# Kernel tuning notes

Measured on AMD Instinct MI355X. Metric: run time of the kernel, lower is better.

The kernel has to match this reference:

```python
import jax, jax.numpy as jnp
import numpy as np

B, C, H, W = 8, 512, 64, 64
HID = 4 * C  # MixFFN hidden = in_dim*4
FOCUS = 3.0


def _ln(x, g, b, eps=1e-5):
    m = x.mean(-1, keepdims=True)
    v = ((x - m) ** 2).mean(-1, keepdims=True)
    return (x - m) / jnp.sqrt(v + eps) * g + b


def setup_inputs() -> dict:
    key = jax.random.key(0)
    ks = jax.random.split(key, 12)
    init = lambda k, shape, fan: (jax.random.normal(k, shape, jnp.float32) / np.float32(np.sqrt(fan)))
    d = {}
    d['x'] = jax.random.normal(ks[0], (B, C, H, W), jnp.float32)
    # 1x1 conv weights stored as (Cout, Cin)
    d['Wq'] = init(ks[1], (C, C), C); d['bq'] = jnp.zeros((C,), jnp.float32)
    d['Wk'] = init(ks[2], (C, C), C); d['bk'] = jnp.zeros((C,), jnp.float32)
    d['Wv'] = init(ks[3], (C, C), C); d['bv'] = jnp.zeros((C,), jnp.float32)
    d['scale'] = jnp.zeros((1, 1, C), jnp.float32)  # nn.Parameter(torch.zeros)
    # MixFFN_skip params
    d['fc1_w'] = init(ks[4], (C, HID), C); d['fc1_b'] = jnp.zeros((HID,), jnp.float32)
    d['dw_w'] = init(ks[5], (HID, 1, 3, 3), 9); d['dw_b'] = jnp.zeros((HID,), jnp.float32)
    d['fc2_w'] = init(ks[6], (HID, C), HID); d['fc2_b'] = jnp.zeros((C,), jnp.float32)
    d['ln1_g'] = jnp.ones((HID,), jnp.float32); d['ln1_b'] = jnp.zeros((HID,), jnp.float32)
    d['lnm_g'] = jnp.ones((C,), jnp.float32); d['lnm_b'] = jnp.zeros((C,), jnp.float32)
    return d


def _forward(x, Wq, bq, Wk, bk, Wv, bv, scale, fc1_w, fc1_b, dw_w, dw_b, fc2_w, fc2_b, ln1_g, ln1_b, lnm_g, lnm_b):
    b, c, h, w = x.shape
    n = h * w
    # 1x1 convs (NCHW), then RAW reshape to (B, N, C) as in torch (no permute!)
    conv1 = lambda t, Wm, bm: jnp.einsum('bchw,oc->bohw', t, Wm) + bm[None, :, None, None]
    q = jax.nn.softmax(conv1(x, Wq, bq).reshape(b, n, c), axis=1)
    k = jax.nn.softmax(conv1(x, Wk, bk).reshape(b, n, c), axis=2)
    v = conv1(x, Wv, bv).reshape(b, n, c)
    q = jax.nn.relu(q) + 1e-6
    k = jax.nn.relu(k) + 1e-6
    sc = jax.nn.softplus(scale)
    q = q / sc
    k = k / sc
    q_norm = jnp.linalg.norm(q, axis=-1, keepdims=True)
    k_norm = jnp.linalg.norm(k, axis=-1, keepdims=True)
    q = q ** FOCUS  # focusing_factor <= 6 branch
    k = k ** FOCUS
    q = q / jnp.linalg.norm(q, axis=-1, keepdims=True) * q_norm
    k = k / jnp.linalg.norm(k, axis=-1, keepdims=True) * k_norm
    # num_heads == 1: (b h) n c == b n c
    z = 1.0 / (jnp.einsum('bic,bc->bi', q, k.sum(axis=1)) + 1e-6)
    kv = jnp.einsum('bjc,bjd->bcd', k, v)  # O(N) linear attention summary
    attn = jnp.einsum('bic,bcd,bi->bid', q, kv, z)
    shortcut = jnp.transpose(x, (0, 2, 3, 1)).reshape(b, n, c)  # proper rearrange b c h w -> b (h w) c
    enhanced = shortcut + attn
    # MixFFN_skip(norm_mlp(enhanced), h, w)
    t = _ln(enhanced, lnm_g, lnm_b)
    a = t @ fc1_w + fc1_b  # (B, N, HID)
    ai = jnp.transpose(a, (0, 2, 1)).reshape(b, HID, h, w)
    dw = jax.lax.conv_general_dilated(ai, dw_w, (1, 1), 'SAME',
                                      dimension_numbers=('NCHW', 'OIHW', 'NCHW'),
                                      feature_group_count=HID)
    dw = dw + dw_b[None, :, None, None]
    dw = jnp.transpose(dw.reshape(b, HID, n), (0, 2, 1))
    ax = jax.nn.gelu(_ln(dw + a, ln1_g, ln1_b), approximate=False)
    mlp_out = ax @ fc2_w + fc2_b
    out = enhanced + mlp_out
    return out.reshape(b, h, w, c)


def reference(x, Wq, bq, Wk, bk, Wv, bv, scale, fc1_w, fc1_b, dw_w, dw_b, fc2_w, fc2_b, ln1_g, ln1_b, lnm_g, lnm_b):
    return _forward(x, Wq, bq, Wk, bk, Wv, bv, scale, fc1_w, fc1_b, dw_w, dw_b, fc2_w, fc2_b, ln1_g, ln1_b, lnm_g, lnm_b)
```

## Files before the change

### kernel.cpp

```cpp
#include <hip/hip_runtime.h>
#include <hip/hip_bf16.h>

typedef __hip_bfloat16 bf16;
typedef __attribute__((ext_vector_type(8))) short bh8;
typedef __attribute__((ext_vector_type(4))) short bh4;
typedef __attribute__((ext_vector_type(4))) float f32x4;

#define CDIM 512
#define NDIM 4096
#define HIDD 2048
#define BATCH 8

__device__ __forceinline__ float bf2f(short s) {
    union { unsigned u; float f; } c; c.u = ((unsigned)(unsigned short)s) << 16; return c.f;
}
__device__ __forceinline__ short f2bf(float f) {
    union { __hip_bfloat16 h; short s; } c; c.h = __float2bfloat16(f); return c.s;
}
__device__ __forceinline__ float wsum(float v) {
#pragma unroll
    for (int o = 32; o; o >>= 1) v += __shfl_xor(v, o);
    return v;
}
__device__ __forceinline__ float wmax(float v) {
#pragma unroll
    for (int o = 32; o; o >>= 1) v = fmaxf(v, __shfl_xor(v, o));
    return v;
}

#define GLL(g, l) __builtin_amdgcn_global_load_lds( \
    (const __attribute__((address_space(1))) unsigned int*)(g), \
    (__attribute__((address_space(3))) unsigned int*)(l), 16, 0, 0)

__device__ __forceinline__ void xcd_swz(int& bx, int& by, int& bz) {
    const int gx = gridDim.x, gy = gridDim.y;
    const int nwg = gx * gy * gridDim.z;
    int lid = blockIdx.x + gx * (blockIdx.y + gy * blockIdx.z);
    const int cpx = nwg >> 3;
    int swz = (lid & 7) * cpx + (lid >> 3);
    bx = swz % gx; swz /= gx;
    by = swz % gy;
    bz = swz / gy;
}

enum { EP_QEXP = 0, EP_BF16_BROW = 1, EP_ATTN = 3, EP_BF16_BCOL = 4, EP_OUT = 5 };

template<int MODE, int TM>
__global__ __launch_bounds__(256)
void gemm_bt(const bf16* __restrict__ A, int lda, long sA,
             const bf16* __restrict__ Bt, int ldb, long sB,
             void* __restrict__ Cp, int ldc, long sC, int K,
             const float* __restrict__ bias,
             const float* __restrict__ aux1, long sAux1,
             const float* __restrict__ aux2, long sAux2)
{
    constexpr int MF = TM / 32;
    __shared__ __align__(16) bf16 As[TM * 64];
    __shared__ __align__(16) bf16 Bs[128 * 64];
    int bx, by, bz;
    xcd_swz(bx, by, bz);
    const bf16* Ab = A + (long)bz * sA + (long)by * TM * lda;
    const bf16* Bb = Bt + (long)bz * sB + (long)bx * 128 * ldb;
    const int t = threadIdx.x, lane = t & 63, wid = t >> 6;
    const int wm = wid >> 1, wn = wid & 1, lg = lane >> 4, lr = lane & 15;

    f32x4 acc[MF][4];
#pragma unroll
    for (int m = 0; m < MF; ++m)
#pragma unroll
        for (int n = 0; n < 4; ++n) acc[m][n] = (f32x4){0.f, 0.f, 0.f, 0.f};

    for (int kt = 0; kt < K; kt += 64) {
#pragma unroll
        for (int i = 0; i < MF; ++i) {
            const int ch = i * 256 + t;
            const int row = ch >> 3;
            const int cs = (ch & 7) ^ (row & 7);
            GLL(Ab + (long)row * lda + kt + (cs << 3), (char*)As + i * 4096 + wid * 1024);
        }
#pragma unroll
        for (int i = 0; i < 4; ++i) {
            const int ch = i * 256 + t;
            const int row = ch >> 3;
            const int cs = (ch & 7) ^ (row & 7);
            GLL(Bb + (long)row * ldb + kt + (cs << 3), (char*)Bs + i * 4096 + wid * 1024);
        }
        __syncthreads();
#pragma unroll
        for (int kk = 0; kk < 2; ++kk) {
            bh8 af[MF], bfv[4];
#pragma unroll
            for (int m = 0; m < MF; ++m) {
                const int row = wm * (TM / 2) + m * 16 + lr;
                const int kc = (kk * 4 + lg) ^ (row & 7);
                af[m] = *(const bh8*)(As + row * 64 + kc * 8);
            }
#pragma unroll
            for (int n = 0; n < 4; ++n) {
                const int row = wn * 64 + n * 16 + lr;
                const int kc = (kk * 4 + lg) ^ (row & 7);
                bfv[n] = *(const bh8*)(Bs + row * 64 + kc * 8);
            }
#pragma unroll
            for (int m = 0; m < MF; ++m)
#pragma unroll
                for (int n = 0; n < 4; ++n)
                    acc[m][n] = __builtin_amdgcn_mfma_f32_16x16x32_bf16(af[m], bfv[n], acc[m][n], 0, 0, 0);
        }
        __syncthreads();
    }

    const int gr0 = by * TM + wm * (TM / 2);
    const int gc0 = bx * 128 + wn * 64;
#pragma unroll
    for (int m = 0; m < MF; ++m) {
#pragma unroll
        for (int n = 0; n < 4; ++n) {
            const int gc = gc0 + n * 16 + lr;
#pragma unroll
            for (int r = 0; r < 4; ++r) {
                const int gr = gr0 + m * 16 + lg * 4 + r;
                float v = acc[m][n][r];
                if constexpr (MODE == EP_QEXP) {
                    ((bf16*)Cp + (long)bz * sC)[(long)gr * ldc + gc] = __float2bfloat16(expf(v + bias[gr]));
                } else if constexpr (MODE == EP_BF16_BROW) {
                    ((bf16*)Cp + (long)bz * sC)[(long)gr * ldc + gc] = __float2bfloat16(v + bias[gr]);
                } else if constexpr (MODE == EP_ATTN) {
                    const float* xg = aux1 + (long)bz * sAux1;
                    const float* zg = aux2 + (long)bz * sAux2;
                    ((float*)Cp + (long)bz * sC)[(long)gr * ldc + gc] = zg[gr] * v + xg[(long)gc * NDIM + gr];
                } else if constexpr (MODE == EP_BF16_BCOL) {
                    ((bf16*)Cp + (long)bz * sC)[(long)gr * ldc + gc] = __float2bfloat16(v + bias[gc]);
                } else {
                    float* op = (float*)Cp;
                    const long idx = (long)gr * ldc + gc;
                    op[idx] = v + bias[gc] + aux1[idx];
                }
            }
        }
    }
}

__global__ __launch_bounds__(256)
void gemm_tn_splitk(const bf16* __restrict__ A, int lda, long sA,
                    const bf16* __restrict__ B, int ldb, long sB,
                    float* __restrict__ part)
{
    __shared__ __align__(16) short As[64 * 128];
    __shared__ __align__(16) short Bs[64 * 128];
    int bx, by, bzl;
    xcd_swz(bx, by, bzl);
    const int bz = bzl >> 2, ks = bzl & 3;
    const bf16* Ab = A + (long)bz * sA + (long)ks * 1024 * lda + by * 128;
    const bf16* Bb = B + (long)bz * sB + (long)ks * 1024 * ldb + bx * 128;
    const int t = threadIdx.x, lane = t & 63, wid = t >> 6;
    const int wm = wid >> 1, wn = wid & 1, lg = lane >> 4, lr = lane & 15;

    f32x4 acc[4][4];
#pragma unroll
    for (int m = 0; m < 4; ++m)
#pragma unroll
        for (int n = 0; n < 4; ++n) acc[m][n] = (f32x4){0.f, 0.f, 0.f, 0.f};

    for (int kt = 0; kt < 1024; kt += 64) {
#pragma unroll
        for (int i = 0; i < 4; ++i) {
            const int ch = i * 256 + t;
            const int row = ch >> 4;
            const int cs = (ch & 15) ^ (((row >> 3) & 3) << 1);
            GLL(Ab + (long)(kt + row) * lda + (cs << 3), (char*)As + i * 4096 + wid * 1024);
            GLL(Bb + (long)(kt + row) * ldb + (cs << 3), (char*)Bs + i * 4096 + wid * 1024);
        }
        __syncthreads();
#pragma unroll
        for (int kk = 0; kk < 2; ++kk) {
            bh8 af[4], bfv[4];
#pragma unroll
            for (int m = 0; m < 4; ++m) {
                const int col = wm * 64 + m * 16 + lr;
#pragma unroll
                for (int u = 0; u < 8; ++u) {
                    const int row = kk * 32 + lg * 8 + u;
                    af[m][u] = As[row * 128 + (((col >> 3) ^ (((row >> 3) & 3) << 1)) << 3) + (col & 7)];
                }
            }
#pragma unroll
            for (int n = 0; n < 4; ++n) {
                const int col = wn * 64 + n * 16 + lr;
#pragma unroll
                for (int u = 0; u < 8; ++u) {
                    const int row = kk * 32 + lg * 8 + u;
                    bfv[n][u] = Bs[row * 128 + (((col >> 3) ^ (((row >> 3) & 3) << 1)) << 3) + (col & 7)];
                }
            }
#pragma unroll
            for (int m = 0; m < 4; ++m)
#pragma unroll
                for (int n = 0; n < 4; ++n)
                    acc[m][n] = __builtin_amdgcn_mfma_f32_16x16x32_bf16(af[m], bfv[n], acc[m][n], 0, 0, 0);
        }
        __syncthreads();
    }

    float* po = part + ((long)bzl << 18);
    const int gr0 = by * 128 + wm * 64;
    const int gc0 = bx * 128 + wn * 64;
#pragma unroll
    for (int m = 0; m < 4; ++m)
#pragma unroll
        for (int n = 0; n < 4; ++n) {
            const int gc = gc0 + n * 16 + lr;
#pragma unroll
            for (int r = 0; r < 4; ++r) {
                const int gr = gr0 + m * 16 + lg * 4 + r;
                po[(long)gr * 512 + gc] = acc[m][n][r];
            }
        }
}

__global__ __launch_bounds__(256)
void k_kvred(const float* __restrict__ part, bf16* __restrict__ kvt)
{
    const long e = ((long)blockIdx.x * 256 + threadIdx.x) * 4;
    const int b = (int)(e >> 18);
    const int off = (int)(e & 262143);
    f32x4 s = (f32x4){0.f, 0.f, 0.f, 0.f};
#pragma unroll
    for (int ks = 0; ks < 4; ++ks) {
        f32x4 v = *(const f32x4*)(part + (((long)(b * 4 + ks)) << 18) + off);
        s = s + v;
    }
    bh4 o;
#pragma unroll
    for (int j = 0; j < 4; ++j) o[j] = f2bf(s[j]);
    *(bh4*)(kvt + ((long)b << 18) + off) = o;
}

__global__ __launch_bounds__(256)
void k_transpose(const float* __restrict__ src, bf16* __restrict__ dst,
                 int Rd, int Cd, long sSrc, long sDst)
{
    __shared__ float tile[64][65];
    const float* s = src + (long)blockIdx.z * sSrc;
    bf16* d = dst + (long)blockIdx.z * sDst;
    const int r0 = blockIdx.x * 64, c0 = blockIdx.y * 64;
    const int t = threadIdx.x;
#pragma unroll 4
    for (int i = 0; i < 16; ++i) {
        int idx = i * 256 + t;
        int a = idx >> 6, b = idx & 63;
        tile[a][b] = s[(long)(c0 + a) * Rd + r0 + b];
    }
    __syncthreads();
#pragma unroll 4
    for (int i = 0; i < 16; ++i) {
        int idx = i * 256 + t;
        int a = idx >> 6, b = idx & 63;
        d[(long)(r0 + a) * Cd + c0 + b] = __float2bfloat16(tile[b][a]);
    }
}

__global__ void k_cvt_bf16(const float* __restrict__ in, bf16* __restrict__ out, int n) {
    int i = blockIdx.x * 256 + threadIdx.x;
    if (i < n) out[i] = __float2bfloat16(in[i]);
}

__global__ void k_invsc(const float* __restrict__ scale, float* __restrict__ invsc) {
    int j = threadIdx.x;
    invsc[j] = 1.0f / log1pf(expf(scale[j]));
}

__global__ void k_fill(float* o, int n, float v) {
    int i = blockIdx.x * 256 + threadIdx.x; if (i < n) o[i] = v;
}

__global__ void k_dwT(const float* __restrict__ w, float* __restrict__ wT) {
    int i = blockIdx.x * 256 + threadIdx.x;
    if (i < HIDD * 9) {
        int chn = i / 9, kk = i % 9;
        wT[kk * HIDD + chn] = w[i];
    }
}

__global__ __launch_bounds__(256)
void k_qcol_partial(const bf16* __restrict__ qe, float* __restrict__ qpart) {
    const int j = blockIdx.x * 256 + threadIdx.x;
    const int ic = blockIdx.y, b = blockIdx.z;
    const bf16* p = qe + (long)b * (NDIM * CDIM) + (long)ic * 256 * CDIM + j;
    float s = 0.f;
    for (int i = 0; i < 256; ++i) s += bf2f(*(const short*)(p + (long)i * CDIM));
    qpart[((long)b * 16 + ic) * CDIM + j] = s;
}
__global__ __launch_bounds__(256)
void k_qcol_reduce(const float* __restrict__ qpart, float* __restrict__ qsum) {
    const int idx = blockIdx.x * 256 + threadIdx.x;
    const int b = idx >> 9, j = idx & 511;
    float s = 0.f;
#pragma unroll
    for (int ic = 0; ic < 16; ++ic) s += qpart[((long)b * 16 + ic) * CDIM + j];
    qsum[idx] = s;
}

__global__ __launch_bounds__(256)
void k_qrow(const bf16* __restrict__ qe, const float* __restrict__ qsum,
            const float* __restrict__ invsc, bf16* __restrict__ qb)
{
    const long row = (long)blockIdx.x * 4 + (threadIdx.x >> 6);
    const int lane = threadIdx.x & 63;
    const int b = (int)(row >> 12);
    bh8 ev = *(const bh8*)(qe + row * CDIM + lane * 8);
    const float* qs = qsum + b * CDIM + lane * 8;
    const float* is = invsc + lane * 8;
    f32x4 s0 = *(const f32x4*)qs, s1 = *(const f32x4*)(qs + 4);
    f32x4 i0 = *(const f32x4*)is, i1 = *(const f32x4*)(is + 4);
    float q[8];
#pragma unroll
    for (int k = 0; k < 4; ++k) {
        q[k]     = (bf2f(ev[k]) / s0[k] + 1e-6f) * i0[k];
        q[k + 4] = (bf2f(ev[k + 4]) / s1[k] + 1e-6f) * i1[k];
    }
    float s2 = 0.f, s6 = 0.f, q3[8];
#pragma unroll
    for (int k = 0; k < 8; ++k) { s2 += q[k] * q[k]; float c = q[k] * q[k] * q[k]; q3[k] = c; s6 += c * c; }
    s2 = wsum(s2); s6 = wsum(s6);
    const float sc = sqrtf(s2) / sqrtf(s6);
    bh8 o;
#pragma unroll
    for (int k = 0; k < 8; ++k) o[k] = f2bf(q3[k] * sc);
    *(bh8*)(qb + row * CDIM + lane * 8) = o;
}

__global__ __launch_bounds__(256)
void k_krow(bf16* __restrict__ kb, const float* __restrict__ invsc)
{
    const long row = (long)blockIdx.x * 4 + (threadIdx.x >> 6);
    const int lane = threadIdx.x & 63;
    bh8 v = *(const bh8*)(kb + row * CDIM + lane * 8);
    const float* is = invsc + lane * 8;
    f32x4 i0 = *(const f32x4*)is, i1 = *(const f32x4*)(is + 4);
    float xv[8];
#pragma unroll
    for (int k = 0; k < 8; ++k) xv[k] = bf2f(v[k]);
    float mx = -1e30f;
#pragma unroll
    for (int k = 0; k < 8; ++k) mx = fmaxf(mx, xv[k]);
    mx = wmax(mx);
    float e[8], se = 0.f;
#pragma unroll
    for (int k = 0; k < 8; ++k) { e[k] = expf(xv[k] - mx); se += e[k]; }
    se = wsum(se);
    const float inv = 1.0f / se;
    float q[8];
#pragma unroll
    for (int k = 0; k < 4; ++k) {
        q[k]     = (e[k] * inv + 1e-6f) * i0[k];
        q[k + 4] = (e[k + 4] * inv + 1e-6f) * i1[k];
    }
    float s2 = 0.f, s6 = 0.f, q3[8];
#pragma unroll
    for (int k = 0; k < 8; ++k) { s2 += q[k] * q[k]; float c = q[k] * q[k] * q[k]; q3[k] = c; s6 += c * c; }
    s2 = wsum(s2); s6 = wsum(s6);
    const float sc = sqrtf(s2) / sqrtf(s6);
    bh8 o;
#pragma unroll
    for (int k = 0; k < 8; ++k) o[k] = f2bf(q3[k] * sc);
    *(bh8*)(kb + row * CDIM + lane * 8) = o;
}

__global__ __launch_bounds__(256)
void k_colsum_part(const bf16* __restrict__ kb, float* __restrict__ part) {
    const int b = blockIdx.y, jc = blockIdx.x, t = threadIdx.x;
    const bf16* p = kb + (long)b * (NDIM * CDIM) + (long)jc * 256 * CDIM + t * 2;
    float s0 = 0.f, s1 = 0.f;
    for (int j = 0; j < 256; ++j) {
        unsigned u = *(const unsigned*)(p + (long)j * CDIM);
        s0 += bf2f((short)(u & 0xffff));
        s1 += bf2f((short)(u >> 16));
    }
    float* o = part + ((long)b * 16 + jc) * CDIM + t * 2;
    o[0] = s0; o[1] = s1;
}
__global__ __launch_bounds__(256)
void k_colsum_red(const float* __restrict__ part, float* __restrict__ ksum) {
    const int idx = blockIdx.x * 256 + threadIdx.x;
    const int b = idx >> 9, c = idx & 511;
    float s = 0.f;
#pragma unroll
    for (int jc = 0; jc < 16; ++jc) s += part[((long)b * 16 + jc) * CDIM + c];
    ksum[idx] = s;
}

__global__ __launch_bounds__(256)
void k_z(const bf16* __restrict__ qb, const float* __restrict__ ksum, float* __restrict__ z)
{
    const long row = (long)blockIdx.x * 4 + (threadIdx.x >> 6);
    const int lane = threadIdx.x & 63;
    const int b = (int)(row >> 12);
    bh8 q = *(const bh8*)(qb + row * CDIM + lane * 8);
    const float* ks = ksum + (long)b * CDIM + lane * 8;
    f32x4 k0 = *(const f32x4*)ks, k1 = *(const f32x4*)(ks + 4);
    float s = 0.f;
#pragma unroll
    for (int j = 0; j < 4; ++j) { s += bf2f(q[j]) * k0[j]; s += bf2f(q[j + 4]) * k1[j]; }
    s = wsum(s);
    if (lane == 0) z[row] = 1.0f / (s + 1e-6f);
}

__global__ __launch_bounds__(256)
void k_ln512(const float* __restrict__ src, const float* __restrict__ g,
             const float* __restrict__ bta, bf16* __restrict__ dst)
{
    const long row = (long)blockIdx.x * 4 + (threadIdx.x >> 6);
    const int lane = threadIdx.x & 63;
    const float* p = src + row * CDIM + lane * 8;
    f32x4 a0 = *(const f32x4*)p, a1 = *(const f32x4*)(p + 4);
    float s = 0.f, ss = 0.f;
#pragma unroll
    for (int k = 0; k < 4; ++k) { s += a0[k] + a1[k]; ss += a0[k] * a0[k] + a1[k] * a1[k]; }
    s = wsum(s); ss = wsum(ss);
    const float mean = s * (1.0f / 512), var = ss * (1.0f / 512) - mean * mean;
    const float rstd = rsqrtf(var + 1e-5f);
    const float* gp = g + lane * 8;
    const float* bp = bta + lane * 8;
    f32x4 g0 = *(const f32x4*)gp, g1 = *(const f32x4*)(gp + 4);
    f32x4 b0 = *(const f32x4*)bp, b1 = *(const f32x4*)(bp + 4);
    bh8 o;
#pragma unroll
    for (int k = 0; k < 4; ++k) {
        o[k]     = f2bf((a0[k] - mean) * rstd * g0[k] + b0[k]);
        o[k + 4] = f2bf((a1[k] - mean) * rstd * g1[k] + b1[k]);
    }
    *(bh8*)(dst + row * CDIM + lane * 8) = o;
}

__global__ __launch_bounds__(256)
void k_dwlngelu4(const bf16* __restrict__ a, const float* __restrict__ dwwT,
                 const float* __restrict__ dwb, const float* __restrict__ g1,
                 const float* __restrict__ b1, bf16* __restrict__ ax)
{
    const long s0 = (long)blockIdx.x * 4;
    const int h = (int)((s0 >> 6) & 63);
    const int w0 = (int)(s0 & 63);
    const int ch = threadIdx.x * 8;

    float wgt[9][8];
#pragma unroll
    for (int kk = 0; kk < 9; ++kk) {
        f32x4 w0v = *(const f32x4*)(dwwT + kk * HIDD + ch);
        f32x4 w1v = *(const f32x4*)(dwwT + kk * HIDD + ch + 4);
#pragma unroll
        for (int j = 0; j < 4; ++j) { wgt[kk][j] = w0v[j]; wgt[kk][j + 4] = w1v[j]; }
    }
#pragma unroll
    for (int j = 0; j < 8; ++j) wgt[4][j] += 1.0f;

    float acc[4][8];
    {
        f32x4 d0 = *(const f32x4*)(dwb + ch), d1 = *(const f32x4*)(dwb + ch + 4);
#pragma unroll
        for (int ti = 0; ti < 4; ++ti)
#pragma unroll
            for (int j = 0; j < 4; ++j) { acc[ti][j] = d0[j]; acc[ti][j + 4] = d1[j]; }
    }

#pragma unroll
    for (int dy = -1; dy <= 1; ++dy) {
        const int hh = h + dy;
        if ((unsigned)hh >= 64u) continue;
#pragma unroll
        for (int c = -1; c <= 4; ++c) {
            const int ww = w0 + c;
            if ((unsigned)ww >= 64u) continue;
            bh8 v = *(const bh8*)(a + (s0 + (long)dy * 64 + c) * HIDD + ch);
            float f[8];
#pragma unroll
            for (int j = 0; j < 8; ++j) f[j] = bf2f(v[j]);
#pragma unroll
            for (int ti = 0; ti < 4; ++ti) {
                const int dx = c - ti;
                if (dx < -1 || dx > 1) continue;
                const int kk = (dy + 1) * 3 + (dx + 1);
#pragma unroll
                for (int j = 0; j < 8; ++j) acc[ti][j] += wgt[kk][j] * f[j];
            }
        }
    }

    float sv[4], qv[4];
#pragma unroll
    for (int ti = 0; ti < 4; ++ti) {
        float s = 0.f, q = 0.f;
#pragma unroll
        for (int j = 0; j < 8; ++j) { s += acc[ti][j]; q += acc[ti][j] * acc[ti][j]; }
        sv[ti] = wsum(s); qv[ti] = wsum(q);
    }
    __shared__ float red[4][4][2];
    const int wid = threadIdx.x >> 6, lane = threadIdx.x & 63;
    if (lane == 0)
#pragma unroll
        for (int ti = 0; ti < 4; ++ti) { red[wid][ti][0] = sv[ti]; red[wid][ti][1] = qv[ti]; }
    __syncthreads();

    f32x4 ga = *(const f32x4*)(g1 + ch), gb = *(const f32x4*)(g1 + ch + 4);
    f32x4 ba = *(const f32x4*)(b1 + ch), bb = *(const f32x4*)(b1 + ch + 4);
    float gg[8], bb8[8];
#pragma unroll
    for (int j = 0; j < 4; ++j) { gg[j] = ga[j]; gg[j + 4] = gb[j]; bb8[j] = ba[j]; bb8[j + 4] = bb[j]; }

#pragma unroll
    for (int ti = 0; ti < 4; ++ti) {
        const float s = red[0][ti][0] + red[1][ti][0] + red[2][ti][0] + red[3][ti][0];
        const float q = red[0][ti][1] + red[1][ti][1] + red[2][ti][1] + red[3][ti][1];
        const float mean = s * (1.0f / 2048), var = q * (1.0f / 2048) - mean * mean;
        const float rstd = rsqrtf(var + 1e-5f);
        bh8 o;
#pragma unroll
        for (int j = 0; j < 8; ++j) {
            float y = (acc[ti][j] - mean) * rstd * gg[j] + bb8[j];
            o[j] = f2bf(0.5f * y * (1.0f + erff(y * 0.70710678118654752f)));
        }
        *(bh8*)(ax + (s0 + ti) * HIDD + ch) = o;
    }
}

extern "C" void kernel_launch(void* const* d_in, const int* in_sizes, int n_in,
                              void* d_out, int out_size, void* d_ws, size_t ws_size,
                              hipStream_t stream) {
    const float* x     = (const float*)d_in[0];
    const float* Wq    = (const float*)d_in[1];
    const float* bq    = (const float*)d_in[2];
    const float* Wk    = (const float*)d_in[3];
    const float* bk    = (const float*)d_in[4];
    const float* Wv    = (const float*)d_in[5];
    const float* bv    = (const float*)d_in[6];
    const float* scale = (const float*)d_in[7];
    const float* fc1_w = (const float*)d_in[8];
    const float* fc1_b = (const float*)d_in[9];
    const float* dw_w  = (const float*)d_in[10];
    const float* dw_b  = (const float*)d_in[11];
    const float* fc2_w = (const float*)d_in[12];
    const float* fc2_b = (const float*)d_in[13];
    const float* ln1_g = (const float*)d_in[14];
    const float* ln1_b = (const float*)d_in[15];
    const float* lnm_g = (const float*)d_in[16];
    const float* lnm_b = (const float*)d_in[17];
    float* out = (float*)d_out;
    char* p = (char*)d_ws;

    bf16*  xbT   = (bf16*)(p + 0);
    bf16*  kb    = (bf16*)(p + 33554432);
    bf16*  vb    = (bf16*)(p + 67108864);
    bf16*  kvt   = (bf16*)(p + 100663296);
    bf16*  wqb   = (bf16*)(p + 104857600);
    bf16*  wkb   = (bf16*)(p + 105381888);
    bf16*  wvb   = (bf16*)(p + 105906176);
    bf16*  fc1wT = (bf16*)(p + 106430464);
    bf16*  fc2wT = (bf16*)(p + 108527616);
    float* invsc = (float*)(p + 110624768);
    float* dwwT  = (float*)(p + 110626816);
    float* qsum  = (float*)(p + 110757888);
    float* kpartX= (float*)(p + 110774272);
    float* ksum  = (float*)(p + 110905344);
    float* zbuf  = (float*)(p + 110921728);
    const size_t REQUIRED = 111052800;
    float* qpart = (float*)kvt;
    float* kpart = (float*)((char*)kvt + 262144);
    bf16*  qe    = (bf16*)out;
    bf16*  qb    = xbT;
    bf16*  abuf  = (bf16*)(p + 0);
    bf16*  axbuf = (bf16*)(p + 33554432);
    bf16*  tbuf  = (bf16*)(p + 67108864);

    if (ws_size < REQUIRED) {
        k_fill<<<(out_size + 255) / 256, 256, 0, stream>>>(out, out_size, 100000.0f + (float)(ws_size >> 20));
        return;
    }
    (void)kpartX;

    const long NC = (long)NDIM * CDIM;

    k_cvt_bf16<<<1024, 256, 0, stream>>>(Wq, wqb, 262144);
    k_cvt_bf16<<<1024, 256, 0, stream>>>(Wk, wkb, 262144);
    k_cvt_bf16<<<1024, 256, 0, stream>>>(Wv, wvb, 262144);
    k_transpose<<<dim3(32, 8, 1), 256, 0, stream>>>(fc1_w, fc1wT, 2048, 512, 0, 0);
    k_transpose<<<dim3(8, 32, 1), 256, 0, stream>>>(fc2_w, fc2wT, 512, 2048, 0, 0);
    k_invsc<<<1, 512, 0, stream>>>(scale, invsc);
    k_transpose<<<dim3(64, 8, BATCH), 256, 0, stream>>>(x, xbT, 4096, 512, NC, NC);

    gemm_bt<EP_QEXP, 128><<<dim3(32, 4, 8), 256, 0, stream>>>(wqb, 512, 0, xbT, 512, NC, qe, 4096, NC, 512, bq, nullptr, 0, nullptr, 0);
    gemm_bt<EP_BF16_BROW, 128><<<dim3(32, 4, 8), 256, 0, stream>>>(wkb, 512, 0, xbT, 512, NC, kb, 4096, NC, 512, bk, nullptr, 0, nullptr, 0);
    gemm_bt<EP_BF16_BROW, 128><<<dim3(32, 4, 8), 256, 0, stream>>>(wvb, 512, 0, xbT, 512, NC, vb, 4096, NC, 512, bv, nullptr, 0, nullptr, 0);

    k_qcol_partial<<<dim3(2, 16, 8), 256, 0, stream>>>(qe, qpart);
    k_qcol_reduce<<<16, 256, 0, stream>>>(qpart, qsum);
    k_qrow<<<8192, 256, 0, stream>>>(qe, qsum, invsc, qb);
    k_krow<<<8192, 256, 0, stream>>>(kb, invsc);
    k_colsum_part<<<dim3(16, 8), 256, 0, stream>>>(kb, kpart);
    k_colsum_red<<<16, 256, 0, stream>>>(kpart, ksum);
    k_z<<<8192, 256, 0, stream>>>(qb, ksum, zbuf);

    gemm_tn_splitk<<<dim3(4, 4, 32), 256, 0, stream>>>(vb, 512, NC, kb, 512, NC, out);
    k_kvred<<<2048, 256, 0, stream>>>(out, kvt);
    gemm_bt<EP_ATTN, 128><<<dim3(4, 32, 8), 256, 0, stream>>>(qb, 512, NC, kvt, 512, 262144, out, 512, NC, 512, nullptr, x, NC, zbuf, 4096);

    k_dwT<<<72, 256, 0, stream>>>(dw_w, dwwT);
    k_ln512<<<8192, 256, 0, stream>>>(out, lnm_g, lnm_b, tbuf);
    for (int q4 = 0; q4 < 4; ++q4) {
        float* outq = out + (long)q4 * 8192 * CDIM;
        bf16* tq = tbuf + (long)q4 * 8192 * CDIM;
        gemm_bt<EP_BF16_BCOL, 128><<<dim3(16, 64, 1), 256, 0, stream>>>(tq, 512, 0, fc1wT, 512, 0, abuf, 2048, 0, 512, fc1_b, nullptr, 0, nullptr, 0);
        k_dwlngelu4<<<2048, 256, 0, stream>>>(abuf, dwwT, dw_b, ln1_g, ln1_b, axbuf);
        gemm_bt<EP_OUT, 64><<<dim3(4, 128, 1), 256, 0, stream>>>(axbuf, 2048, 0, fc2wT, 2048, 0, outq, 512, 0, 2048, fc2_b, outq, 0, nullptr, 0);
    }
}
```

Measured before the change: 670.2 us.

## Fuse prep/reduction kernels, compute z in qrow, bf16 kv partials and shortcut

Merges the three weight conversions into one launch, folds invsc and depthwise-weight transpose into one prep kernel, and combines the q and k column-sum reductions into a single kernel. The z normalizer is computed inside k_qrow instead of a separate pass that re-reads qb. Split-K kv partials are stored as bf16, which halves their traffic, and the attention epilogue reads the shortcut from the transposed bf16 xbT row-major instead of strided fp32 x. The trade is lower precision in the kv partial sums and the residual shortcut, plus buffer aliasing that had to be reshuffled (qb now lives in kb, kv partials in out).

Result: faster. 640.4 us (-4.5%).

```diff
diff --git a/kernel.cpp b/kernel.cpp
--- a/kernel.cpp
+++ b/kernel.cpp
@@ -51,7 +51,7 @@
              const bf16* __restrict__ Bt, int ldb, long sB,
              void* __restrict__ Cp, int ldc, long sC, int K,
              const float* __restrict__ bias,
-             const float* __restrict__ aux1, long sAux1,
+             const void* __restrict__ aux1, long sAux1,
              const float* __restrict__ aux2, long sAux2)
 {
     constexpr int MF = TM / 32;
@@ -126,15 +126,16 @@
                 } else if constexpr (MODE == EP_BF16_BROW) {
                     ((bf16*)Cp + (long)bz * sC)[(long)gr * ldc + gc] = __float2bfloat16(v + bias[gr]);
                 } else if constexpr (MODE == EP_ATTN) {
-                    const float* xg = aux1 + (long)bz * sAux1;
+                    const bf16* xg = (const bf16*)aux1 + (long)bz * sAux1;
                     const float* zg = aux2 + (long)bz * sAux2;
-                    ((float*)Cp + (long)bz * sC)[(long)gr * ldc + gc] = zg[gr] * v + xg[(long)gc * NDIM + gr];
+                    ((float*)Cp + (long)bz * sC)[(long)gr * ldc + gc] =
+                        zg[gr] * v + bf2f(*(const short*)(xg + (long)gr * 512 + gc));
                 } else if constexpr (MODE == EP_BF16_BCOL) {
                     ((bf16*)Cp + (long)bz * sC)[(long)gr * ldc + gc] = __float2bfloat16(v + bias[gc]);
                 } else {
                     float* op = (float*)Cp;
                     const long idx = (long)gr * ldc + gc;
-                    op[idx] = v + bias[gc] + aux1[idx];
+                    op[idx] = v + bias[gc] + ((const float*)aux1)[idx];
                 }
             }
         }
@@ -144,7 +145,7 @@
 __global__ __launch_bounds__(256)
 void gemm_tn_splitk(const bf16* __restrict__ A, int lda, long sA,
                     const bf16* __restrict__ B, int ldb, long sB,
-                    float* __restrict__ part)
+                    bf16* __restrict__ part)
 {
     __shared__ __align__(16) short As[64 * 128];
     __shared__ __align__(16) short Bs[64 * 128];
@@ -202,7 +203,7 @@
         __syncthreads();
     }
 
-    float* po = part + ((long)bzl << 18);
+    bf16* po = part + ((long)bzl << 18);
     const int gr0 = by * 128 + wm * 64;
     const int gc0 = bx * 128 + wn * 64;
 #pragma unroll
@@ -213,27 +214,28 @@
 #pragma unroll
             for (int r = 0; r < 4; ++r) {
                 const int gr = gr0 + m * 16 + lg * 4 + r;
-                po[(long)gr * 512 + gc] = acc[m][n][r];
+                po[(long)gr * 512 + gc] = __float2bfloat16(acc[m][n][r]);
             }
         }
 }
 
 __global__ __launch_bounds__(256)
-void k_kvred(const float* __restrict__ part, bf16* __restrict__ kvt)
-{
-    const long e = ((long)blockIdx.x * 256 + threadIdx.x) * 4;
+void k_kvred(const bf16* __restrict__ part, bf16* __restrict__ kvt)
+{
+    const long e = ((long)blockIdx.x * 256 + threadIdx.x) * 8;
     const int b = (int)(e >> 18);
     const int off = (int)(e & 262143);
-    f32x4 s = (f32x4){0.f, 0.f, 0.f, 0.f};
+    float s[8] = {0.f, 0.f, 0.f, 0.f, 0.f, 0.f, 0.f, 0.f};
 #pragma unroll
     for (int ks = 0; ks < 4; ++ks) {
-        f32x4 v = *(const f32x4*)(part + (((long)(b * 4 + ks)) << 18) + off);
-        s = s + v;
-    }
-    bh4 o;
-#pragma unroll
-    for (int j = 0; j < 4; ++j) o[j] = f2bf(s[j]);
-    *(bh4*)(kvt + ((long)b << 18) + off) = o;
+        bh8 v = *(const bh8*)(part + (((long)(b * 4 + ks)) << 18) + off);
+#pragma unroll
+        for (int j = 0; j < 8; ++j) s[j] += bf2f(v[j]);
+    }
+    bh8 o;
+#pragma unroll
+    for (int j = 0; j < 8; ++j) o[j] = f2bf(s[j]);
+    *(bh8*)(kvt + ((long)b << 18) + off) = o;
 }
 
 __global__ __launch_bounds__(256)
@@ -260,26 +262,29 @@
     }
 }
 
-__global__ void k_cvt_bf16(const float* __restrict__ in, bf16* __restrict__ out, int n) {
+__global__ void k_cvt3(const float* __restrict__ a, const float* __restrict__ b,
+                       const float* __restrict__ c, bf16* __restrict__ oa,
+                       bf16* __restrict__ ob, bf16* __restrict__ oc) {
     int i = blockIdx.x * 256 + threadIdx.x;
-    if (i < n) out[i] = __float2bfloat16(in[i]);
-}
-
-__global__ void k_invsc(const float* __restrict__ scale, float* __restrict__ invsc) {
-    int j = threadIdx.x;
-    invsc[j] = 1.0f / log1pf(expf(scale[j]));
-}
-
-__global__ void k_fill(float* o, int n, float v) {
-    int i = blockIdx.x * 256 + threadIdx.x; if (i < n) o[i] = v;
-}
-
-__global__ void k_dwT(const float* __restrict__ w, float* __restrict__ wT) {
+    if (i < 262144) {
+        oa[i] = __float2bfloat16(a[i]);
+        ob[i] = __float2bfloat16(b[i]);
+        oc[i] = __float2bfloat16(c[i]);
+    }
+}
+
+__global__ void k_prep(const float* __restrict__ scale, float* __restrict__ invsc,
+                       const float* __restrict__ w, float* __restrict__ wT) {
     int i = blockIdx.x * 256 + threadIdx.x;
+    if (i < 512) invsc[i] = 1.0f / log1pf(expf(scale[i]));
     if (i < HIDD * 9) {
         int chn = i / 9, kk = i % 9;
         wT[kk * HIDD + chn] = w[i];
     }
+}
+
+__global__ void k_fill(float* o, int n, float v) {
+    int i = blockIdx.x * 256 + threadIdx.x; if (i < n) o[i] = v;
 }
 
 __global__ __launch_bounds__(256)
@@ -291,19 +296,24 @@
     for (int i = 0; i < 256; ++i) s += bf2f(*(const short*)(p + (long)i * CDIM));
     qpart[((long)b * 16 + ic) * CDIM + j] = s;
 }
-__global__ __launch_bounds__(256)
-void k_qcol_reduce(const float* __restrict__ qpart, float* __restrict__ qsum) {
+
+__global__ __launch_bounds__(256)
+void k_red2(const float* __restrict__ qpart, float* __restrict__ qsum,
+            const float* __restrict__ kpart, float* __restrict__ ksum) {
     const int idx = blockIdx.x * 256 + threadIdx.x;
-    const int b = idx >> 9, j = idx & 511;
+    const int which = idx >> 12, r = idx & 4095;
+    const int b = r >> 9, c = r & 511;
+    const float* src = which ? kpart : qpart;
     float s = 0.f;
 #pragma unroll
-    for (int ic = 0; ic < 16; ++ic) s += qpart[((long)b * 16 + ic) * CDIM + j];
-    qsum[idx] = s;
+    for (int jc = 0; jc < 16; ++jc) s += src[((long)(b * 16 + jc)) * CDIM + c];
+    (which ? ksum : qsum)[r] = s;
 }
 
 __global__ __launch_bounds__(256)
 void k_qrow(const bf16* __restrict__ qe, const float* __restrict__ qsum,
-            const float* __restrict__ invsc, bf16* __restrict__ qb)
+            const float* __restrict__ invsc, bf16* __restrict__ qb,
+            const float* __restrict__ ksum, float* __restrict__ z)
 {
     const long row = (long)blockIdx.x * 4 + (threadIdx.x >> 6);
     const int lane = threadIdx.x & 63;
@@ -328,6 +338,13 @@
 #pragma unroll
     for (int k = 0; k < 8; ++k) o[k] = f2bf(q3[k] * sc);
     *(bh8*)(qb + row * CDIM + lane * 8) = o;
+    const float* ks = ksum + (long)b * CDIM + lane * 8;
+    f32x4 k0 = *(const f32x4*)ks, k1 = *(const f32x4*)(ks + 4);
+    float zd = 0.f;
+#pragma unroll
+    for (int j = 0; j < 4; ++j) { zd += bf2f(o[j]) * k0[j]; zd += bf2f(o[j + 4]) * k1[j]; }
+    zd = wsum(zd);
+    if (lane == 0) z[row] = 1.0f / (zd + 1e-6f);
 }
 
 __global__ __launch_bounds__(256)
@@ -379,31 +396,6 @@
     }
     float* o = part + ((long)b * 16 + jc) * CDIM + t * 2;
     o[0] = s0; o[1] = s1;
-}
-__global__ __launch_bounds__(256)
-void k_colsum_red(const float* __restrict__ part, float* __restrict__ ksum) {
-    const int idx = blockIdx.x * 256 + threadIdx.x;
-    const int b = idx >> 9, c = idx & 511;
-    float s = 0.f;
-#pragma unroll
-    for (int jc = 0; jc < 16; ++jc) s += part[((long)b * 16 + jc) * CDIM + c];
-    ksum[idx] = s;
-}
-
-__global__ __launch_bounds__(256)
-void k_z(const bf16* __restrict__ qb, const float* __restrict__ ksum, float* __restrict__ z)
-{
-    const long row = (long)blockIdx.x * 4 + (threadIdx.x >> 6);
-    const int lane = threadIdx.x & 63;
-    const int b = (int)(row >> 12);
-    bh8 q = *(const bh8*)(qb + row * CDIM + lane * 8);
-    const float* ks = ksum + (long)b * CDIM + lane * 8;
-    f32x4 k0 = *(const f32x4*)ks, k1 = *(const f32x4*)(ks + 4);
-    float s = 0.f;
-#pragma unroll
-    for (int j = 0; j < 4; ++j) { s += bf2f(q[j]) * k0[j]; s += bf2f(q[j + 4]) * k1[j]; }
-    s = wsum(s);
-    if (lane == 0) z[row] = 1.0f / (s + 1e-6f);
 }
 
 __global__ __launch_bounds__(256)
@@ -559,14 +551,14 @@
     float* invsc = (float*)(p + 110624768);
     float* dwwT  = (float*)(p + 110626816);
     float* qsum  = (float*)(p + 110757888);
-    float* kpartX= (float*)(p + 110774272);
     float* ksum  = (float*)(p + 110905344);
     float* zbuf  = (float*)(p + 110921728);
     const size_t REQUIRED = 111052800;
     float* qpart = (float*)kvt;
     float* kpart = (float*)((char*)kvt + 262144);
     bf16*  qe    = (bf16*)out;
-    bf16*  qb    = xbT;
+    bf16*  kvpart= (bf16*)((char*)out + 33554432);
+    bf16*  qb    = kb;
     bf16*  abuf  = (bf16*)(p + 0);
     bf16*  axbuf = (bf16*)(p + 33554432);
     bf16*  tbuf  = (bf16*)(p + 67108864);
@@ -575,16 +567,13 @@
         k_fill<<<(out_size + 255) / 256, 256, 0, stream>>>(out, out_size, 100000.0f + (float)(ws_size >> 20));
         return;
     }
-    (void)kpartX;
 
     const long NC = (long)NDIM * CDIM;
 
-    k_cvt_bf16<<<1024, 256, 0, stream>>>(Wq, wqb, 262144);
-    k_cvt_bf16<<<1024, 256, 0, stream>>>(Wk, wkb, 262144);
-    k_cvt_bf16<<<1024, 256, 0, stream>>>(Wv, wvb, 262144);
+    k_cvt3<<<1024, 256, 0, stream>>>(Wq, Wk, Wv, wqb, wkb, wvb);
     k_transpose<<<dim3(32, 8, 1), 256, 0, stream>>>(fc1_w, fc1wT, 2048, 512, 0, 0);
     k_transpose<<<dim3(8, 32, 1), 256, 0, stream>>>(fc2_w, fc2wT, 512, 2048, 0, 0);
-    k_invsc<<<1, 512, 0, stream>>>(scale, invsc);
+    k_prep<<<72, 256, 0, stream>>>(scale, invsc, dw_w, dwwT);
     k_transpose<<<dim3(64, 8, BATCH), 256, 0, stream>>>(x, xbT, 4096, 512, NC, NC);
 
     gemm_bt<EP_QEXP, 128><<<dim3(32, 4, 8), 256, 0, stream>>>(wqb, 512, 0, xbT, 512, NC, qe, 4096, NC, 512, bq, nullptr, 0, nullptr, 0);
@@ -592,18 +581,17 @@
     gemm_bt<EP_BF16_BROW, 128><<<dim3(32, 4, 8), 256, 0, stream>>>(wvb, 512, 0, xbT, 512, NC, vb, 4096, NC, 512, bv, nullptr, 0, nullptr, 0);
 
     k_qcol_partial<<<dim3(2, 16, 8), 256, 0, stream>>>(qe, qpart);
-    k_qcol_reduce<<<16, 256, 0, stream>>>(qpart, qsum);
-    k_qrow<<<8192, 256, 0, stream>>>(qe, qsum, invsc, qb);
     k_krow<<<8192, 256, 0, stream>>>(kb, invsc);
     k_colsum_part<<<dim3(16, 8), 256, 0, stream>>>(kb, kpart);
-    k_colsum_red<<<16, 256, 0, stream>>>(kpart, ksum);
-    k_z<<<8192, 256, 0, stream>>>(qb, ksum, zbuf);
-
-    gemm_tn_splitk<<<dim3(4, 4, 32), 256, 0, stream>>>(vb, 512, NC, kb, 512, NC, out);
-    k_kvred<<<2048, 256, 0, stream>>>(out, kvt);
-    gemm_bt<EP_ATTN, 128><<<dim3(4, 32, 8), 256, 0, stream>>>(qb, 512, NC, kvt, 512, 262144, out, 512, NC, 512, nullptr, x, NC, zbuf, 4096);
-
-    k_dwT<<<72, 256, 0, stream>>>(dw_w, dwwT);
+    k_red2<<<32, 256, 0, stream>>>(qpart, qsum, kpart, ksum);
+
+    gemm_tn_splitk<<<dim3(4, 4, 32), 256, 0, stream>>>(vb, 512, NC, kb, 512, NC, kvpart);
+    k_kvred<<<1024, 256, 0, stream>>>(kvpart, kvt);
+
+    k_qrow<<<8192, 256, 0, stream>>>(qe, qsum, invsc, qb, ksum, zbuf);
+
+    gemm_bt<EP_ATTN, 128><<<dim3(4, 32, 8), 256, 0, stream>>>(qb, 512, NC, kvt, 512, 262144, out, 512, NC, 512, nullptr, xbT, NC, zbuf, 4096);
+
     k_ln512<<<8192, 256, 0, stream>>>(out, lnm_g, lnm_b, tbuf);
     for (int q4 = 0; q4 < 4; ++q4) {
         float* outq = out + (long)q4 * 8192 * CDIM;
```
